# Kernel tuning notes

Hardware: AMD Instinct MI355X
Metric: run time of the kernel (lower is better)

The kernel has to match this reference:

```python
import jax, jax.numpy as jnp
import numpy as np

N, E, G = 50000, 800000, 64   # nodes, edges, graphs
F, H, O = 6, 256, 2           # in_dim, hidden_dim, out_dim
NE, K, L = 8, 2, 4            # n_experts, top_k, n_layers


def setup_inputs() -> dict:
    key = jax.random.key(0)
    ks = jax.random.split(key, 12)
    s = 0.05
    return {
        "x": jax.random.normal(ks[0], (N, F), jnp.float32),
        "edge_index": jax.random.randint(ks[1], (2, E), 0, N),
        "batch": jnp.sort(jax.random.randint(ks[2], (N,), 0, G)),
        "enc_W": jax.random.normal(ks[3], (F, H), jnp.float32) * s,
        "enc_b": jnp.zeros((H,), jnp.float32),
        "rtr_W1": jax.random.normal(ks[4], (H + 2, H), jnp.float32) * s,
        "rtr_b1": jnp.zeros((H,), jnp.float32),
        "rtr_W2": jax.random.normal(ks[5], (H, NE), jnp.float32) * s,
        "rtr_b2": jnp.zeros((NE,), jnp.float32),
        "hid_Wr": jax.random.normal(ks[6], (L - 1, NE, H, H), jnp.float32) * s,
        "hid_Wn": jax.random.normal(ks[7], (L - 1, NE, H, H), jnp.float32) * s,
        "hid_b": jnp.zeros((L - 1, NE, H), jnp.float32),
        "out_Wr": jax.random.normal(ks[8], (NE, H, O), jnp.float32) * s,
        "out_Wn": jax.random.normal(ks[9], (NE, H, O), jnp.float32) * s,
        "out_b": jnp.zeros((NE, O), jnp.float32),
    }


def reference(x, edge_index, batch, enc_W, enc_b, rtr_W1, rtr_b1, rtr_W2, rtr_b2,
              hid_Wr, hid_Wn, hid_b, out_Wr, out_Wn, out_b):
    src, dst = edge_index[0], edge_index[1]

    # SharedBusEncoder: Linear + ReLU
    h = jax.nn.relu(x @ enc_W + enc_b)  # [N, H]

    # graph_size_features: per-graph node/edge counts, log-scaled, per node
    ones_n = jnp.ones((N,), h.dtype)
    nodes_per_g = jax.ops.segment_sum(ones_n, batch, num_segments=G)
    edges_per_g = jax.ops.segment_sum(jnp.ones((E,), h.dtype), batch[src], num_segments=G)
    size_feat = jnp.stack([jnp.log(nodes_per_g + 1.0)[batch],
                           jnp.log(edges_per_g + 1.0)[batch]], axis=-1)  # [N, 2]

    # BaseRouter: 2-layer MLP -> logits [N, NE]
    r = jax.nn.relu(jnp.concatenate([h, size_feat], axis=-1) @ rtr_W1 + rtr_b1)
    logits = r @ rtr_W2 + rtr_b2

    # sparse_routing (eval mode): softmax over top-k logits, scattered to dense mask
    vals, idx = jax.lax.top_k(logits, K)  # [N, K]
    w = jax.nn.softmax(vals, axis=-1)
    sparse = jnp.zeros((N, NE), h.dtype).at[jnp.arange(N)[:, None], idx].set(w)

    # Dense all-expert GraphConv stacks, mask-sum combine
    def graph_conv(he, Wr, Wn, b):
        agg = jax.ops.segment_sum(he[src], dst, num_segments=N)  # sum-aggregate neighbors
        return he @ Wr + agg @ Wn + b

    out = jnp.zeros((N, O), h.dtype)
    for e in range(NE):
        he = h
        for l in range(L - 1):
            he = jax.nn.relu(graph_conv(he, hid_Wr[l, e], hid_Wn[l, e], hid_b[l, e]))
        ye = graph_conv(he, out_Wr[e], out_Wn[e], out_b[e])  # [N, O]
        out = out + ye * sparse[:, e:e + 1]
    return out
```

## Files before the change

kernel.cpp:

```cpp
#include <hip/hip_runtime.h>
#include <cstdint>

#define NN 50000
#define EE 800000
#define GG 64

typedef unsigned short u16;
typedef __attribute__((ext_vector_type(8))) short bf16x8;
typedef __attribute__((ext_vector_type(4))) float f32x4;

__device__ __forceinline__ float bf2f(u16 v) { return __uint_as_float(((unsigned)v) << 16); }
__device__ __forceinline__ u16 f2bf(float f) {
  unsigned u = __float_as_uint(f);
  return (u16)((u + 0x7fffu + ((u >> 16) & 1u)) >> 16);
}

__device__ __forceinline__ void gload_lds16(const void* g, void* l) {
  __builtin_amdgcn_global_load_lds(
      (const __attribute__((address_space(1))) void*)g,
      (__attribute__((address_space(3))) void*)l,
      16, 0, 0);
}

__global__ void k_sentinel(float* out) { out[threadIdx.x] = 1e12f; }

__global__ __launch_bounds__(256) void k_encoder(
    const float* __restrict__ x, const float* __restrict__ W,
    const float* __restrict__ b, u16* __restrict__ hb) {
  int idx = blockIdx.x * 256 + threadIdx.x;
  if (idx >= NN * 256) return;
  int row = idx >> 8, j = idx & 255;
  float s = b[j];
#pragma unroll
  for (int k = 0; k < 6; ++k) s += x[row * 6 + k] * W[k * 256 + j];
  hb[idx] = f2bf(fmaxf(s, 0.f));
}

__global__ __launch_bounds__(256) void k_hist(const int* __restrict__ ei,
                                              int* __restrict__ deg,
                                              int* __restrict__ outdeg) {
  int i = blockIdx.x * 256 + threadIdx.x;
  if (i < EE) {
    atomicAdd(&outdeg[ei[i]], 1);
    atomicAdd(&deg[ei[EE + i]], 1);
  }
}

__global__ __launch_bounds__(256) void k_graph_feats(const int* __restrict__ batch,
                                                     const int* __restrict__ outdeg,
                                                     float* __restrict__ gf) {
  __shared__ int red[256];
  int g = blockIdx.x, tid = threadIdx.x;
  auto lb = [&](int v) {
    int lo = 0, hi = NN;
    while (lo < hi) { int m = (lo + hi) >> 1; if (batch[m] < v) lo = m + 1; else hi = m; }
    return lo;
  };
  int bs = lb(g), be = lb(g + 1);
  int s = 0;
  for (int i = bs + tid; i < be; i += 256) s += outdeg[i];
  red[tid] = s;
  __syncthreads();
  for (int off = 128; off > 0; off >>= 1) {
    if (tid < off) red[tid] += red[tid + off];
    __syncthreads();
  }
  if (tid == 0) {
    gf[g * 2] = logf((float)(be - bs) + 1.f);
    gf[g * 2 + 1] = logf((float)red[0] + 1.f);
  }
}

__global__ __launch_bounds__(256) void k_router(
    const float* __restrict__ x, const float* __restrict__ encW, const float* __restrict__ encb,
    const int* __restrict__ batch, const float* __restrict__ gf,
    const float* __restrict__ W1, const float* __restrict__ b1,
    const float* __restrict__ W2, const float* __restrict__ b2,
    float* __restrict__ sparse) {
  __shared__ __align__(16) float hs_t[258][8];
  __shared__ __align__(16) float rs_t[256][8];
  __shared__ float part2[4][64];
  __shared__ float xv[8][6];
  __shared__ float sf[8][2];
  __shared__ float lg[8][8];
  int tid = threadIdx.x;
  int nb = blockIdx.x * 8;
  if (tid < 48) {
    int r = tid / 6, k = tid % 6;
    int node = nb + r;
    xv[r][k] = (node < NN) ? x[node * 6 + k] : 0.f;
  }
  if (tid >= 48 && tid < 56) {
    int r = tid - 48;
    int node = nb + r;
    int g = (node < NN) ? batch[node] : 0;
    sf[r][0] = gf[g * 2];
    sf[r][1] = gf[g * 2 + 1];
  }
  __syncthreads();
  {
    float wcol[6];
#pragma unroll
    for (int k = 0; k < 6; ++k) wcol[k] = encW[k * 256 + tid];
    float bb = encb[tid];
#pragma unroll
    for (int r = 0; r < 8; ++r) {
      float s = bb;
#pragma unroll
      for (int k = 0; k < 6; ++k) s += xv[r][k] * wcol[k];
      hs_t[tid][r] = fmaxf(s, 0.f);
    }
  }
  if (tid < 16) {
    int r = tid >> 1, c = tid & 1;
    hs_t[256 + c][r] = sf[r][c];
  }
  __syncthreads();
  float acc[8];
  {
    float bb = b1[tid];
#pragma unroll
    for (int r = 0; r < 8; ++r) acc[r] = bb;
  }
  int k = 0;
#pragma unroll 4
  for (; k < 256; ++k) {
    float w = W1[k * 256 + tid];
    float4 ha = *(const float4*)&hs_t[k][0];
    float4 hb4 = *(const float4*)&hs_t[k][4];
    acc[0] += ha.x * w; acc[1] += ha.y * w; acc[2] += ha.z * w; acc[3] += ha.w * w;
    acc[4] += hb4.x * w; acc[5] += hb4.y * w; acc[6] += hb4.z * w; acc[7] += hb4.w * w;
  }
  for (; k < 258; ++k) {
    float w = W1[k * 256 + tid];
    float4 ha = *(const float4*)&hs_t[k][0];
    float4 hb4 = *(const float4*)&hs_t[k][4];
    acc[0] += ha.x * w; acc[1] += ha.y * w; acc[2] += ha.z * w; acc[3] += ha.w * w;
    acc[4] += hb4.x * w; acc[5] += hb4.y * w; acc[6] += hb4.z * w; acc[7] += hb4.w * w;
  }
#pragma unroll
  for (int r = 0; r < 8; ++r) rs_t[tid][r] = fmaxf(acc[r], 0.f);
  __syncthreads();
  {
    int pr = tid & 63, pt = tid >> 6;
    int r = pr >> 3, e = pr & 7;
    float s = 0.f;
    int kk0 = pt * 64;
#pragma unroll 4
    for (int kk = kk0; kk < kk0 + 64; ++kk) s += rs_t[kk][r] * W2[kk * 8 + e];
    part2[pt][pr] = s;
  }
  __syncthreads();
  if (tid < 64) {
    int r = tid >> 3, e = tid & 7;
    lg[r][e] = b2[e] + part2[0][tid] + part2[1][tid] + part2[2][tid] + part2[3][tid];
  }
  __syncthreads();
  if (tid < 8) {
    int node = nb + tid;
    if (node < NN) {
      float v1 = lg[tid][0];
      int j1 = 0;
#pragma unroll
      for (int j = 1; j < 8; ++j) {
        float v = lg[tid][j];
        if (v > v1) { v1 = v; j1 = j; }
      }
      float v2 = -1e30f;
      int j2 = 0;
#pragma unroll
      for (int j = 0; j < 8; ++j) {
        if (j == j1) continue;
        float v = lg[tid][j];
        if (v > v2) { v2 = v; j2 = j; }
      }
      float ex = expf(v2 - v1);
      float wa = 1.f / (1.f + ex), wb = ex / (1.f + ex);
      float* sp = sparse + node * 8;
#pragma unroll
      for (int j = 0; j < 8; ++j) sp[j] = 0.f;
      sp[j1] = wa;
      sp[j2] = wb;
    }
  }
}

__global__ __launch_bounds__(1024) void k_scan(const int* __restrict__ deg,
                                               int* __restrict__ rowptr) {
  __shared__ int tmp[1024];
  __shared__ int carry;
  if (threadIdx.x == 0) { carry = 0; rowptr[0] = 0; }
  __syncthreads();
  for (int base = 0; base < NN; base += 1024) {
    int i = base + threadIdx.x;
    int v = (i < NN) ? deg[i] : 0;
    tmp[threadIdx.x] = v;
    __syncthreads();
    for (int off = 1; off < 1024; off <<= 1) {
      int t = (threadIdx.x >= off) ? tmp[threadIdx.x - off] : 0;
      __syncthreads();
      tmp[threadIdx.x] += t;
      __syncthreads();
    }
    if (i < NN) rowptr[i + 1] = carry + tmp[threadIdx.x];
    int last = tmp[1023];
    __syncthreads();
    if (threadIdx.x == 0) carry += last;
    __syncthreads();
  }
}

__global__ __launch_bounds__(256) void k_fill(const int* __restrict__ ei,
                                              const int* __restrict__ rowptr,
                                              int* __restrict__ cursor, int* __restrict__ csrc) {
  int i = blockIdx.x * 256 + threadIdx.x;
  if (i < EE) {
    int s = ei[i], d = ei[EE + i];
    int pos = atomicAdd(&cursor[d], 1);
    csrc[rowptr[d] + pos] = s;
  }
}

__global__ __launch_bounds__(256) void k_spmm256(
    const int* __restrict__ rowptr, const int* __restrict__ csrc,
    const u16* __restrict__ Xb, size_t xs, u16* __restrict__ Yb, size_t ys) {
  const u16* X = Xb + (size_t)blockIdx.y * xs;
  u16* Y = Yb + (size_t)blockIdx.y * ys;
  int wave = threadIdx.x >> 6, lane = threadIdx.x & 63;
  int d = blockIdx.x * 4 + wave;
  if (d >= NN) return;
  int s0 = rowptr[d], s1 = rowptr[d + 1];
  int c4 = lane * 4;
  float a0 = 0.f, a1 = 0.f, a2 = 0.f, a3 = 0.f;
  int i = s0;
  for (; i + 2 <= s1; i += 2) {
    int sa = csrc[i], sb = csrc[i + 1];
    ushort4 va = *(const ushort4*)(X + sa * 256 + c4);
    ushort4 vb = *(const ushort4*)(X + sb * 256 + c4);
    a0 += bf2f(va.x) + bf2f(vb.x);
    a1 += bf2f(va.y) + bf2f(vb.y);
    a2 += bf2f(va.z) + bf2f(vb.z);
    a3 += bf2f(va.w) + bf2f(vb.w);
  }
  if (i < s1) {
    int sa = csrc[i];
    ushort4 va = *(const ushort4*)(X + sa * 256 + c4);
    a0 += bf2f(va.x);
    a1 += bf2f(va.y);
    a2 += bf2f(va.z);
    a3 += bf2f(va.w);
  }
  ushort4 o;
  o.x = f2bf(a0); o.y = f2bf(a1); o.z = f2bf(a2); o.w = f2bf(a3);
  *(ushort4*)(Y + d * 256 + c4) = o;
}

__global__ __launch_bounds__(256) void k_transpose2(const float* __restrict__ Wr,
                                                    const float* __restrict__ Wn,
                                                    u16* __restrict__ WrT,
                                                    u16* __restrict__ WnT) {
  int idx = blockIdx.x * 256 + threadIdx.x;
  if (idx >= 24 * 65536) return;
  int m = idx >> 16, rem = idx & 65535;
  int k = rem >> 8, j = rem & 255;
  int o = (m << 16) + (j << 8) + k;
  WrT[o] = f2bf(Wr[idx]);
  WnT[o] = f2bf(Wn[idx]);
}

__global__ __launch_bounds__(512) void k_gemm(
    const u16* __restrict__ X1b, size_t x1s, const u16* __restrict__ X2b, size_t x2s,
    const u16* __restrict__ W1tb, const u16* __restrict__ W2tb, size_t wst,
    const float* __restrict__ biasb, size_t bst,
    u16* __restrict__ Yb, size_t yst, int relu,
    const float* __restrict__ oWr, const float* __restrict__ oWn, int e0_base,
    float* __restrict__ Y4self, float* __restrict__ Y4nb, int do_out) {
  __shared__ __align__(16) char smem[49152];
  int g = blockIdx.y;
  const u16* X1 = X1b + (size_t)g * x1s;
  const u16* X2 = X2b + (size_t)g * x2s;
  const u16* W1t = W1tb + (size_t)g * wst;
  const u16* W2t = W2tb + (size_t)g * wst;
  const float* bias = biasb + (size_t)g * bst;
  u16* Y = Yb + (size_t)g * yst;
  int tid = threadIdx.x;
  int wave = tid >> 6, lane = tid & 63;
  int l15 = lane & 15, l4 = lane >> 4;
  int m0 = blockIdx.x * 128;
  int wr = wave >> 2, wc = wave & 3;
  const f32x4 fz = {0.f, 0.f, 0.f, 0.f};
  f32x4 acc[4][4];
#pragma unroll
  for (int a = 0; a < 4; ++a)
#pragma unroll
    for (int b = 0; b < 4; ++b) acc[a][b] = fz;

  auto stage = [&](int t) {
    const u16* xs = (t < 8) ? X1 : X2;
    const u16* wsrc = (t < 8) ? W1t : W2t;
    int kb = (t & 7) * 32;
    int half = t & 1;
    {
      int flat = wave * 1024 + lane * 16;
      int row = flat >> 6, colb = flat & 63;
      int scol = colb ^ (((row >> 1) & 3) << 4);
      int gr = m0 + row;
      if (gr > NN - 1) gr = NN - 1;
      gload_lds16(xs + gr * 256 + kb + (scol >> 1), smem + half * 8192 + flat);
    }
#pragma unroll
    for (int q = 0; q < 2; ++q) {
      int flat = q * 8192 + wave * 1024 + lane * 16;
      int row = flat >> 6, colb = flat & 63;
      int scol = colb ^ (((row >> 1) & 3) << 4);
      gload_lds16(wsrc + row * 256 + kb + (scol >> 1), smem + 16384 + half * 16384 + flat);
    }
  };

  stage(0);
  for (int kt = 0; kt < 16; ++kt) {
    if (kt < 15) {
      stage(kt + 1);
      asm volatile("s_waitcnt vmcnt(3)" ::: "memory");
    } else {
      asm volatile("s_waitcnt vmcnt(0)" ::: "memory");
    }
    __builtin_amdgcn_sched_barrier(0);
    __builtin_amdgcn_s_barrier();
    __builtin_amdgcn_sched_barrier(0);
    const char* Ab = smem + (kt & 1) * 8192;
    const char* Bb = smem + 16384 + (kt & 1) * 16384;
    bf16x8 af[4], bfv[4];
#pragma unroll
    for (int mi = 0; mi < 4; ++mi) {
      int r = wr * 64 + mi * 16 + l15;
      af[mi] = *(const bf16x8*)(Ab + r * 64 + ((l4 * 16) ^ (((r >> 1) & 3) << 4)));
    }
#pragma unroll
    for (int nj = 0; nj < 4; ++nj) {
      int c = wc * 64 + nj * 16 + l15;
      bfv[nj] = *(const bf16x8*)(Bb + c * 64 + ((l4 * 16) ^ (((c >> 1) & 3) << 4)));
    }
#pragma unroll
    for (int mi = 0; mi < 4; ++mi)
#pragma unroll
      for (int nj = 0; nj < 4; ++nj)
        acc[mi][nj] =
            __builtin_amdgcn_mfma_f32_16x16x32_bf16(af[mi], bfv[nj], acc[mi][nj], 0, 0, 0);
    __builtin_amdgcn_sched_barrier(0);
    __builtin_amdgcn_s_barrier();
  }

  if (!do_out) {
#pragma unroll
    for (int mi = 0; mi < 4; ++mi) {
      int rbase = m0 + wr * 64 + mi * 16 + l4 * 4;
#pragma unroll
      for (int nj = 0; nj < 4; ++nj) {
        int col = wc * 64 + nj * 16 + l15;
        float bv = bias[col];
#pragma unroll
        for (int r2 = 0; r2 < 4; ++r2) {
          int row = rbase + r2;
          if (row < NN) {
            float v = acc[mi][nj][r2] + bv;
            if (relu) v = fmaxf(v, 0.f);
            Y[row * 256 + col] = f2bf(v);
          }
        }
      }
    }
  } else {
    int eabs = e0_base + g;
    const float2* wr2p = (const float2*)(oWr + (size_t)eabs * 512);
    const float2* wn2p = (const float2*)(oWn + (size_t)eabs * 512);
    float bv[4]; float2 wa[4], wb[4];
#pragma unroll
    for (int nj = 0; nj < 4; ++nj) {
      int col = wc * 64 + nj * 16 + l15;
      bv[nj] = bias[col];
      wa[nj] = wr2p[col];
      wb[nj] = wn2p[col];
    }
    float* y4red = (float*)smem;
#pragma unroll
    for (int mi = 0; mi < 4; ++mi) {
#pragma unroll
      for (int r2 = 0; r2 < 4; ++r2) {
        float p0 = 0.f, p1 = 0.f, p2 = 0.f, p3 = 0.f;
#pragma unroll
        for (int nj = 0; nj < 4; ++nj) {
          float v = fmaxf(acc[mi][nj][r2] + bv[nj], 0.f);
          p0 += v * wa[nj].x; p1 += v * wa[nj].y;
          p2 += v * wb[nj].x; p3 += v * wb[nj].y;
        }
#pragma unroll
        for (int off2 = 1; off2 < 16; off2 <<= 1) {
          p0 += __shfl_xor(p0, off2); p1 += __shfl_xor(p1, off2);
          p2 += __shfl_xor(p2, off2); p3 += __shfl_xor(p3, off2);
        }
        if (l15 == 0) {
          int lr = wr * 64 + mi * 16 + l4 * 4 + r2;
          float* q = y4red + (lr * 4 + wc) * 4;
          q[0] = p0; q[1] = p1; q[2] = p2; q[3] = p3;
        }
      }
    }
    __syncthreads();
    if (tid < 128) {
      int row = m0 + tid;
      if (row < NN) {
        float s0 = 0.f, s1 = 0.f, n0 = 0.f, n1 = 0.f;
#pragma unroll
        for (int w2 = 0; w2 < 4; ++w2) {
          const float* q = y4red + (tid * 4 + w2) * 4;
          s0 += q[0]; s1 += q[1]; n0 += q[2]; n1 += q[3];
        }
        Y4self[row * 16 + eabs * 2] = s0;
        Y4self[row * 16 + eabs * 2 + 1] = s1;
        Y4nb[row * 16 + eabs * 2] = n0;
        Y4nb[row * 16 + eabs * 2 + 1] = n1;
      }
    }
  }
}

__global__ __launch_bounds__(256) void k_combine(
    const int* __restrict__ rowptr, const int* __restrict__ csrc,
    const float* __restrict__ Y4self, const float* __restrict__ Y4nb,
    const float* __restrict__ sparse, const float* __restrict__ ob,
    float* __restrict__ out) {
  int t = blockIdx.x * 256 + threadIdx.x;
  int d = t >> 3, e = t & 7;
  if (d >= NN) return;
  float s0 = Y4self[d * 16 + e * 2], s1 = Y4self[d * 16 + e * 2 + 1];
  float n0 = 0.f, n1 = 0.f;
  for (int i = rowptr[d]; i < rowptr[d + 1]; ++i) {
    int s = csrc[i];
    float2 v = *(const float2*)(Y4nb + s * 16 + e * 2);
    n0 += v.x;
    n1 += v.y;
  }
  float w = sparse[d * 8 + e];
  float t0 = w * (s0 + n0 + ob[e * 2]);
  float t1 = w * (s1 + n1 + ob[e * 2 + 1]);
  t0 += __shfl_xor(t0, 1); t1 += __shfl_xor(t1, 1);
  t0 += __shfl_xor(t0, 2); t1 += __shfl_xor(t1, 2);
  t0 += __shfl_xor(t0, 4); t1 += __shfl_xor(t1, 4);
  if (e == 0) {
    out[d * 2] = t0;
    out[d * 2 + 1] = t1;
  }
}

extern "C" void kernel_launch(void* const* d_in, const int* in_sizes, int n_in,
                              void* d_out, int out_size, void* d_ws, size_t ws_size,
                              hipStream_t stream) {
  const float* x = (const float*)d_in[0];
  const int* ei = (const int*)d_in[1];
  const int* batch = (const int*)d_in[2];
  const float* enc_W = (const float*)d_in[3];
  const float* enc_b = (const float*)d_in[4];
  const float* rW1 = (const float*)d_in[5];
  const float* rb1 = (const float*)d_in[6];
  const float* rW2 = (const float*)d_in[7];
  const float* rb2 = (const float*)d_in[8];
  const float* hid_Wr = (const float*)d_in[9];
  const float* hid_Wn = (const float*)d_in[10];
  const float* hid_b = (const float*)d_in[11];
  const float* out_Wr = (const float*)d_in[12];
  const float* out_Wn = (const float*)d_in[13];
  const float* out_b = (const float*)d_in[14];
  float* out = (float*)d_out;

  char* ws = (char*)d_ws;
  size_t off = 0;
  auto alloc = [&](size_t bytes) -> void* {
    void* p = ws + off;
    off = (off + bytes + 511) & ~(size_t)511;
    return p;
  };
  const size_t HBYTES = (size_t)NN * 256 * 2;
  u16* hb = (u16*)alloc(HBYTES);
  u16* agg0 = (u16*)alloc(HBYTES);
  u16* WrT = (u16*)alloc((size_t)24 * 65536 * 2);
  u16* WnT = (u16*)alloc((size_t)24 * 65536 * 2);
  int* deg = (int*)alloc((size_t)NN * 4);
  int* cursor = (int*)alloc((size_t)NN * 4);
  int* outdeg = (int*)alloc((size_t)NN * 4);
  size_t zero_bytes = (size_t)((char*)(outdeg + NN) - (char*)deg);
  int* rowptr = (int*)alloc((size_t)(NN + 1) * 4);
  int* csrc = (int*)alloc((size_t)EE * 4);
  float* gf = (float*)alloc(GG * 2 * 4);
  float* sparse = (float*)alloc((size_t)NN * 8 * 4);
  float* Y4self = (float*)alloc((size_t)NN * 16 * 4);
  float* Y4nb = (float*)alloc((size_t)NN * 16 * 4);

  size_t rem = (ws_size > off) ? ws_size - off : 0;
  size_t per = 2 * HBYTES + 2048;
  int grp = (rem >= 4 * per) ? 4 : (rem >= 2 * per) ? 2 : (rem >= per) ? 1 : 0;
  if (grp == 0) {
    k_sentinel<<<1, 2, 0, stream>>>(out);
    return;
  }
  u16* heb = (u16*)alloc((size_t)grp * HBYTES);
  u16* aggb = (u16*)alloc((size_t)grp * HBYTES);

  hipMemsetAsync(deg, 0, zero_bytes, stream);

  k_encoder<<<(NN * 256 + 255) / 256, 256, 0, stream>>>(x, enc_W, enc_b, hb);
  k_transpose2<<<(24 * 65536 + 255) / 256, 256, 0, stream>>>(hid_Wr, hid_Wn, WrT, WnT);
  k_hist<<<(EE + 255) / 256, 256, 0, stream>>>(ei, deg, outdeg);
  k_graph_feats<<<GG, 256, 0, stream>>>(batch, outdeg, gf);
  k_scan<<<1, 1024, 0, stream>>>(deg, rowptr);
  k_fill<<<(EE + 255) / 256, 256, 0, stream>>>(ei, rowptr, cursor, csrc);
  k_router<<<NN / 8, 256, 0, stream>>>(x, enc_W, enc_b, batch, gf, rW1, rb1, rW2, rb2, sparse);

  const int GX = (NN + 127) / 128;
  const int SX = (NN + 3) / 4;
  const size_t HS = (size_t)NN * 256;

  k_spmm256<<<dim3(SX, 1), 256, 0, stream>>>(rowptr, csrc, hb, 0, agg0, 0);
  for (int e0 = 0; e0 < 8; e0 += grp) {
    k_gemm<<<dim3(GX, grp), 512, 0, stream>>>(
        hb, 0, agg0, 0, WrT + e0 * 65536, WnT + e0 * 65536, 65536,
        hid_b + e0 * 256, 256, heb, HS, 1, nullptr, nullptr, 0, nullptr, nullptr, 0);
    k_spmm256<<<dim3(SX, grp), 256, 0, stream>>>(rowptr, csrc, heb, HS, aggb, HS);
    k_gemm<<<dim3(GX, grp), 512, 0, stream>>>(
        heb, HS, aggb, HS, WrT + (8 + e0) * 65536, WnT + (8 + e0) * 65536, 65536,
        hid_b + (8 + e0) * 256, 256, heb, HS, 1, nullptr, nullptr, 0, nullptr, nullptr, 0);
    k_spmm256<<<dim3(SX, grp), 256, 0, stream>>>(rowptr, csrc, heb, HS, aggb, HS);
    k_gemm<<<dim3(GX, grp), 512, 0, stream>>>(
        heb, HS, aggb, HS, WrT + (16 + e0) * 65536, WnT + (16 + e0) * 65536, 65536,
        hid_b + (16 + e0) * 256, 256, heb, HS, 1, out_Wr, out_Wn, e0, Y4self, Y4nb, 1);
  }
  k_combine<<<(NN * 8 + 255) / 256, 256, 0, stream>>>(rowptr, csrc, Y4self, Y4nb, sparse,
                                                      out_b, out);
}
```

Before: 2.313 ms.

## Interleave expert activations per node and fuse encoder output into router kernel

Switches the per-expert hidden and aggregate buffers from expert-major to node-major interleaved layout with row stride grp*256. A new SpMM kernel gathers all grouped experts' features for a neighbor in one contiguous row, so each edge's column index is read once for the whole group and the gathers are longer. The router kernel now also writes the bf16 encoder output, which removes the separate encoder kernel. The GEMM gains row-stride parameters, and the bounds guards are dropped because NN is a multiple of 8.

```diff
diff --git a/kernel.cpp b/kernel.cpp
--- a/kernel.cpp
+++ b/kernel.cpp
@@ -23,18 +23,6 @@
 }
 
 __global__ void k_sentinel(float* out) { out[threadIdx.x] = 1e12f; }
-
-__global__ __launch_bounds__(256) void k_encoder(
-    const float* __restrict__ x, const float* __restrict__ W,
-    const float* __restrict__ b, u16* __restrict__ hb) {
-  int idx = blockIdx.x * 256 + threadIdx.x;
-  if (idx >= NN * 256) return;
-  int row = idx >> 8, j = idx & 255;
-  float s = b[j];
-#pragma unroll
-  for (int k = 0; k < 6; ++k) s += x[row * 6 + k] * W[k * 256 + j];
-  hb[idx] = f2bf(fmaxf(s, 0.f));
-}
 
 __global__ __launch_bounds__(256) void k_hist(const int* __restrict__ ei,
                                               int* __restrict__ deg,
@@ -76,7 +64,7 @@
     const int* __restrict__ batch, const float* __restrict__ gf,
     const float* __restrict__ W1, const float* __restrict__ b1,
     const float* __restrict__ W2, const float* __restrict__ b2,
-    float* __restrict__ sparse) {
+    float* __restrict__ sparse, u16* __restrict__ hb_out) {
   __shared__ __align__(16) float hs_t[258][8];
   __shared__ __align__(16) float rs_t[256][8];
   __shared__ float part2[4][64];
@@ -87,13 +75,11 @@
   int nb = blockIdx.x * 8;
   if (tid < 48) {
     int r = tid / 6, k = tid % 6;
-    int node = nb + r;
-    xv[r][k] = (node < NN) ? x[node * 6 + k] : 0.f;
+    xv[r][k] = x[(nb + r) * 6 + k];
   }
   if (tid >= 48 && tid < 56) {
     int r = tid - 48;
-    int node = nb + r;
-    int g = (node < NN) ? batch[node] : 0;
+    int g = batch[nb + r];
     sf[r][0] = gf[g * 2];
     sf[r][1] = gf[g * 2 + 1];
   }
@@ -108,7 +94,9 @@
       float s = bb;
 #pragma unroll
       for (int k = 0; k < 6; ++k) s += xv[r][k] * wcol[k];
-      hs_t[tid][r] = fmaxf(s, 0.f);
+      float h = fmaxf(s, 0.f);
+      hs_t[tid][r] = h;
+      hb_out[(nb + r) * 256 + tid] = f2bf(h);
     }
   }
   if (tid < 16) {
@@ -158,7 +146,7 @@
   __syncthreads();
   if (tid < 8) {
     int node = nb + tid;
-    if (node < NN) {
+    {
       float v1 = lg[tid][0];
       int j1 = 0;
 #pragma unroll
@@ -223,9 +211,7 @@
 
 __global__ __launch_bounds__(256) void k_spmm256(
     const int* __restrict__ rowptr, const int* __restrict__ csrc,
-    const u16* __restrict__ Xb, size_t xs, u16* __restrict__ Yb, size_t ys) {
-  const u16* X = Xb + (size_t)blockIdx.y * xs;
-  u16* Y = Yb + (size_t)blockIdx.y * ys;
+    const u16* __restrict__ X, u16* __restrict__ Y) {
   int wave = threadIdx.x >> 6, lane = threadIdx.x & 63;
   int d = blockIdx.x * 4 + wave;
   if (d >= NN) return;
@@ -255,6 +241,38 @@
   *(ushort4*)(Y + d * 256 + c4) = o;
 }
 
+__global__ __launch_bounds__(256) void k_spmm_intl(
+    const int* __restrict__ rowptr, const int* __restrict__ csrc,
+    const u16* __restrict__ X, u16* __restrict__ Y, int rs) {
+  int d = blockIdx.x;
+  int tid = threadIdx.x;
+  if (tid * 4 >= rs) return;
+  int s0 = rowptr[d], s1 = rowptr[d + 1];
+  int c4 = tid * 4;
+  float a0 = 0.f, a1 = 0.f, a2 = 0.f, a3 = 0.f;
+  int i = s0;
+  for (; i + 2 <= s1; i += 2) {
+    int sa = csrc[i], sb = csrc[i + 1];
+    ushort4 va = *(const ushort4*)(X + (size_t)sa * rs + c4);
+    ushort4 vb = *(const ushort4*)(X + (size_t)sb * rs + c4);
+    a0 += bf2f(va.x) + bf2f(vb.x);
+    a1 += bf2f(va.y) + bf2f(vb.y);
+    a2 += bf2f(va.z) + bf2f(vb.z);
+    a3 += bf2f(va.w) + bf2f(vb.w);
+  }
+  if (i < s1) {
+    int sa = csrc[i];
+    ushort4 va = *(const ushort4*)(X + (size_t)sa * rs + c4);
+    a0 += bf2f(va.x);
+    a1 += bf2f(va.y);
+    a2 += bf2f(va.z);
+    a3 += bf2f(va.w);
+  }
+  ushort4 o;
+  o.x = f2bf(a0); o.y = f2bf(a1); o.z = f2bf(a2); o.w = f2bf(a3);
+  *(ushort4*)(Y + (size_t)d * rs + c4) = o;
+}
+
 __global__ __launch_bounds__(256) void k_transpose2(const float* __restrict__ Wr,
                                                     const float* __restrict__ Wn,
                                                     u16* __restrict__ WrT,
@@ -269,20 +287,21 @@
 }
 
 __global__ __launch_bounds__(512) void k_gemm(
-    const u16* __restrict__ X1b, size_t x1s, const u16* __restrict__ X2b, size_t x2s,
+    const u16* __restrict__ X1b, size_t x1gs, int x1rs,
+    const u16* __restrict__ X2b, size_t x2gs, int x2rs,
     const u16* __restrict__ W1tb, const u16* __restrict__ W2tb, size_t wst,
     const float* __restrict__ biasb, size_t bst,
-    u16* __restrict__ Yb, size_t yst, int relu,
+    u16* __restrict__ Yb, size_t ygs, int yrs, int relu,
     const float* __restrict__ oWr, const float* __restrict__ oWn, int e0_base,
     float* __restrict__ Y4self, float* __restrict__ Y4nb, int do_out) {
   __shared__ __align__(16) char smem[49152];
   int g = blockIdx.y;
-  const u16* X1 = X1b + (size_t)g * x1s;
-  const u16* X2 = X2b + (size_t)g * x2s;
+  const u16* X1 = X1b + (size_t)g * x1gs;
+  const u16* X2 = X2b + (size_t)g * x2gs;
   const u16* W1t = W1tb + (size_t)g * wst;
   const u16* W2t = W2tb + (size_t)g * wst;
   const float* bias = biasb + (size_t)g * bst;
-  u16* Y = Yb + (size_t)g * yst;
+  u16* Y = Yb + (size_t)g * ygs;
   int tid = threadIdx.x;
   int wave = tid >> 6, lane = tid & 63;
   int l15 = lane & 15, l4 = lane >> 4;
@@ -297,6 +316,7 @@
 
   auto stage = [&](int t) {
     const u16* xs = (t < 8) ? X1 : X2;
+    int xrs = (t < 8) ? x1rs : x2rs;
     const u16* wsrc = (t < 8) ? W1t : W2t;
     int kb = (t & 7) * 32;
     int half = t & 1;
@@ -306,7 +326,7 @@
       int scol = colb ^ (((row >> 1) & 3) << 4);
       int gr = m0 + row;
       if (gr > NN - 1) gr = NN - 1;
-      gload_lds16(xs + gr * 256 + kb + (scol >> 1), smem + half * 8192 + flat);
+      gload_lds16(xs + (size_t)gr * xrs + kb + (scol >> 1), smem + half * 8192 + flat);
     }
 #pragma unroll
     for (int q = 0; q < 2; ++q) {
@@ -365,7 +385,7 @@
           if (row < NN) {
             float v = acc[mi][nj][r2] + bv;
             if (relu) v = fmaxf(v, 0.f);
-            Y[row * 256 + col] = f2bf(v);
+            Y[(size_t)row * yrs + col] = f2bf(v);
           }
         }
       }
@@ -505,34 +525,36 @@
   }
   u16* heb = (u16*)alloc((size_t)grp * HBYTES);
   u16* aggb = (u16*)alloc((size_t)grp * HBYTES);
+  const int RS = grp * 256;
 
   hipMemsetAsync(deg, 0, zero_bytes, stream);
 
-  k_encoder<<<(NN * 256 + 255) / 256, 256, 0, stream>>>(x, enc_W, enc_b, hb);
   k_transpose2<<<(24 * 65536 + 255) / 256, 256, 0, stream>>>(hid_Wr, hid_Wn, WrT, WnT);
   k_hist<<<(EE + 255) / 256, 256, 0, stream>>>(ei, deg, outdeg);
   k_graph_feats<<<GG, 256, 0, stream>>>(batch, outdeg, gf);
   k_scan<<<1, 1024, 0, stream>>>(deg, rowptr);
   k_fill<<<(EE + 255) / 256, 256, 0, stream>>>(ei, rowptr, cursor, csrc);
-  k_router<<<NN / 8, 256, 0, stream>>>(x, enc_W, enc_b, batch, gf, rW1, rb1, rW2, rb2, sparse);
+  k_router<<<NN / 8, 256, 0, stream>>>(x, enc_W, enc_b, batch, gf, rW1, rb1, rW2, rb2,
+                                       sparse, hb);
 
   const int GX = (NN + 127) / 128;
-  const int SX = (NN + 3) / 4;
   const size_t HS = (size_t)NN * 256;
-
-  k_spmm256<<<dim3(SX, 1), 256, 0, stream>>>(rowptr, csrc, hb, 0, agg0, 0);
+  (void)HS;
+
+  k_spmm256<<<(NN + 3) / 4, 256, 0, stream>>>(rowptr, csrc, hb, agg0);
   for (int e0 = 0; e0 < 8; e0 += grp) {
     k_gemm<<<dim3(GX, grp), 512, 0, stream>>>(
-        hb, 0, agg0, 0, WrT + e0 * 65536, WnT + e0 * 65536, 65536,
-        hid_b + e0 * 256, 256, heb, HS, 1, nullptr, nullptr, 0, nullptr, nullptr, 0);
-    k_spmm256<<<dim3(SX, grp), 256, 0, stream>>>(rowptr, csrc, heb, HS, aggb, HS);
+        hb, 0, 256, agg0, 0, 256, WrT + e0 * 65536, WnT + e0 * 65536, 65536,
+        hid_b + e0 * 256, 256, heb, 256, RS, 1, nullptr, nullptr, 0, nullptr, nullptr, 0);
+    k_spmm_intl<<<NN, 256, 0, stream>>>(rowptr, csrc, heb, aggb, RS);
     k_gemm<<<dim3(GX, grp), 512, 0, stream>>>(
-        heb, HS, aggb, HS, WrT + (8 + e0) * 65536, WnT + (8 + e0) * 65536, 65536,
-        hid_b + (8 + e0) * 256, 256, heb, HS, 1, nullptr, nullptr, 0, nullptr, nullptr, 0);
-    k_spmm256<<<dim3(SX, grp), 256, 0, stream>>>(rowptr, csrc, heb, HS, aggb, HS);
+        heb, 256, RS, aggb, 256, RS, WrT + (8 + e0) * 65536, WnT + (8 + e0) * 65536, 65536,
+        hid_b + (8 + e0) * 256, 256, heb, 256, RS, 1, nullptr, nullptr, 0, nullptr, nullptr, 0);
+    k_spmm_intl<<<NN, 256, 0, stream>>>(rowptr, csrc, heb, aggb, RS);
     k_gemm<<<dim3(GX, grp), 512, 0, stream>>>(
-        heb, HS, aggb, HS, WrT + (16 + e0) * 65536, WnT + (16 + e0) * 65536, 65536,
-        hid_b + (16 + e0) * 256, 256, heb, HS, 1, out_Wr, out_Wn, e0, Y4self, Y4nb, 1);
+        heb, 256, RS, aggb, 256, RS, WrT + (16 + e0) * 65536, WnT + (16 + e0) * 65536, 65536,
+        hid_b + (16 + e0) * 256, 256, nullptr, 0, 256, 1, out_Wr, out_Wn, e0,
+        Y4self, Y4nb, 1);
   }
   k_combine<<<(NN * 8 + 255) / 256, 256, 0, stream>>>(rowptr, csrc, Y4self, Y4nb, sparse,
                                                       out_b, out);
```

New measurement: 2.249 ms. 2.8% less time.
